# Optimization experiments

Measured on AMD Instinct MI355X. Metric: run time of the kernel, lower is better.

## Reference

```python
import jax, jax.numpy as jnp
import numpy as np

EMBED = 256
HEADS = 8
HEAD_DIM = 32
MLP_DIM = 1024
NEG = -1e9  # large negative in place of -inf so fully-deselected rows don't NaN
LN_EPS = 1e-5


def _layernorm(x, g, b):
    m = jnp.mean(x, axis=-1, keepdims=True)
    v = jnp.mean(jnp.square(x - m), axis=-1, keepdims=True)
    return (x - m) / jnp.sqrt(v + LN_EPS) * g + b


def setup_inputs() -> dict:
    key = jax.random.key(0)
    ks = jax.random.split(key, 16)
    b, s, d = 64, 360, EMBED
    sc = 0.02
    return {
        "x": jax.random.normal(ks[0], (b, s, d), dtype=jnp.float32),
        "attention_mask": jnp.zeros((b, 1, 1, s), dtype=jnp.float32),
        # TokenRouter.weight_predictor: Linear(256, 1)
        "wp_w": jax.random.normal(ks[1], (1, d), dtype=jnp.float32) * sc,
        "wp_b": jnp.zeros((1,), dtype=jnp.float32),
        # TokenRouter.aux_predictor: Linear(256,128) -> SiLU -> Linear(128,2)
        "a1_w": jax.random.normal(ks[2], (d // 2, d), dtype=jnp.float32) * sc,
        "a1_b": jnp.zeros((d // 2,), dtype=jnp.float32),
        "a2_w": jax.random.normal(ks[3], (2, d // 2), dtype=jnp.float32) * sc,
        "a2_b": jnp.zeros((2,), dtype=jnp.float32),
        # transformer block (pre-LN GPT2-style)
        "ln1_g": jnp.ones((d,), dtype=jnp.float32),
        "ln1_b": jnp.zeros((d,), dtype=jnp.float32),
        "wqkv": jax.random.normal(ks[4], (d, 3 * d), dtype=jnp.float32) * sc,
        "bqkv": jnp.zeros((3 * d,), dtype=jnp.float32),
        "wo": jax.random.normal(ks[5], (d, d), dtype=jnp.float32) * sc,
        "bo": jnp.zeros((d,), dtype=jnp.float32),
        "ln2_g": jnp.ones((d,), dtype=jnp.float32),
        "ln2_b": jnp.zeros((d,), dtype=jnp.float32),
        "w1": jax.random.normal(ks[6], (d, MLP_DIM), dtype=jnp.float32) * sc,
        "b1": jnp.zeros((MLP_DIM,), dtype=jnp.float32),
        "w2": jax.random.normal(ks[7], (MLP_DIM, d), dtype=jnp.float32) * sc,
        "b2": jnp.zeros((d,), dtype=jnp.float32),
    }


def reference(x, attention_mask, wp_w, wp_b, a1_w, a1_b, a2_w, a2_b,
              ln1_g, ln1_b, wqkv, bqkv, wo, bo, ln2_g, ln2_b, w1, b1, w2, b2):
    b, s, d = x.shape
    # --- router: per-token scalar weight ---
    weights = (x @ wp_w.T + wp_b).squeeze(-1)  # [b, s]
    # --- aux predictor selects tokens (eval path: argmax over 2 logits) ---
    h = jax.nn.silu(x @ a1_w.T + a1_b)
    aux_logits = h @ a2_w.T + a2_b            # [b, s, 2]
    sel = jnp.argmax(aux_logits, axis=-1).astype(bool)  # [b, s]
    # --- masked transformer block over the selected token subset.
    # Compacting tokens then attending == full-seq attention with deselected
    # keys masked out (LN/MLP/residual are position-wise), so vectorize:
    bias = attention_mask + jnp.where(sel, 0.0, NEG)[:, None, None, :]  # [b,1,1,s]
    hn = _layernorm(x, ln1_g, ln1_b)
    qkv = hn @ wqkv + bqkv
    q, k, v = jnp.split(qkv, 3, axis=-1)
    q = q.reshape(b, s, HEADS, HEAD_DIM)
    k = k.reshape(b, s, HEADS, HEAD_DIM)
    v = v.reshape(b, s, HEADS, HEAD_DIM)
    scores = jnp.einsum("bqhd,bkhd->bhqk", q, k) / np.sqrt(HEAD_DIM).astype(np.float32)
    scores = scores + bias                   # [b, h, s, s]
    attn = jax.nn.softmax(scores, axis=-1)
    ctx = jnp.einsum("bhqk,bkhd->bqhd", attn, v).reshape(b, s, d)
    h1 = x + (ctx @ wo + bo)
    h2n = _layernorm(h1, ln2_g, ln2_b)
    block_out = h1 + (jax.nn.gelu(h2n @ w1 + b1) @ w2 + b2)  # [b, s, d]
    # --- scatter-recombine: selected -> weighted block output, else passthrough
    out = jnp.where(sel[..., None], block_out * weights[..., None], x)
    avg_selected = jnp.sum(sel.astype(x.dtype)) / b
    return out, avg_selected
```

## Files before the change

kernel.cpp:

```cpp
#include <hip/hip_runtime.h>
#include <math.h>
#include <stdint.h>

#define TOKN 23040
#define BSZ 64
#define SEQ 360
#define DIM 256
#define NHD 8
#define HDD 32
#define MLPD 1024
#define NEGV -1e9f

typedef __attribute__((ext_vector_type(8))) short bf16x8;
typedef __attribute__((ext_vector_type(4))) float f32x4;

static __device__ __forceinline__ short f2bs(float f) {
  unsigned u = __builtin_bit_cast(unsigned, f);
  u += 0x7fffu + ((u >> 16) & 1u);
  return (short)(u >> 16);
}
static __device__ __forceinline__ float bf2f(short s) {
  unsigned u = ((unsigned)(unsigned short)s) << 16;
  return __builtin_bit_cast(float, u);
}
static __device__ __forceinline__ unsigned packbf(float a, float b) {
  return (unsigned)(unsigned short)f2bs(a) | ((unsigned)(unsigned short)f2bs(b) << 16);
}
static __device__ __forceinline__ void gl16(const short* g, short* l) {
  __builtin_amdgcn_global_load_lds(
      (const __attribute__((address_space(1))) unsigned int*)g,
      (__attribute__((address_space(3))) unsigned int*)l, 16, 0, 0);
}

__global__ __launch_bounds__(256) void convw_k(
    const float* __restrict__ wqkv, const float* __restrict__ wo,
    const float* __restrict__ w1, const float* __restrict__ w2,
    short* __restrict__ wqkvt, short* __restrict__ wot,
    short* __restrict__ w1t, short* __restrict__ w2t) {
  __shared__ float tile[32][33];
  int bid = blockIdx.x;
  const float* src;
  short* dst;
  int K, N, kt, nt;
  if (bid < 192) {
    src = wqkv; dst = wqkvt; K = 256; N = 768; kt = bid / 24; nt = bid % 24;
  } else if (bid < 256) {
    int b = bid - 192; src = wo; dst = wot; K = 256; N = 256; kt = b >> 3; nt = b & 7;
  } else if (bid < 512) {
    int b = bid - 256; src = w1; dst = w1t; K = 256; N = 1024; kt = b >> 5; nt = b & 31;
  } else {
    int b = bid - 512; src = w2; dst = w2t; K = 1024; N = 256; kt = b >> 3; nt = b & 7;
  }
  int t = threadIdx.x, r = t >> 3, c4 = (t & 7) * 4;
  const float4 v = *(const float4*)(src + (size_t)(kt * 32 + r) * N + nt * 32 + c4);
  tile[c4 + 0][r] = v.x;
  tile[c4 + 1][r] = v.y;
  tile[c4 + 2][r] = v.z;
  tile[c4 + 3][r] = v.w;
  __syncthreads();
  union { short s[4]; uint2 u; } o;
  o.s[0] = f2bs(tile[r][c4 + 0]);
  o.s[1] = f2bs(tile[r][c4 + 1]);
  o.s[2] = f2bs(tile[r][c4 + 2]);
  o.s[3] = f2bs(tile[r][c4 + 3]);
  *(uint2*)(dst + (size_t)(nt * 32 + r) * K + kt * 32 + c4) = o.u;
}

__global__ __launch_bounds__(256) void ln_router_k(
    const float* __restrict__ in, const float* __restrict__ g,
    const float* __restrict__ b, const float* __restrict__ wpw,
    const float* __restrict__ wpb, short* __restrict__ outn,
    float* __restrict__ wout, float* __restrict__ outx) {
  int tok = blockIdx.x * 4 + (threadIdx.x >> 6);
  int lane = threadIdx.x & 63;
  const float4 xv = *(const float4*)(in + (size_t)tok * DIM + lane * 4);
  *(float4*)(outx + (size_t)tok * DIM + lane * 4) = xv;
  float s = xv.x + xv.y + xv.z + xv.w;
  float s2 = xv.x * xv.x + xv.y * xv.y + xv.z * xv.z + xv.w * xv.w;
#pragma unroll
  for (int o = 1; o < 64; o <<= 1) { s += __shfl_xor(s, o); s2 += __shfl_xor(s2, o); }
  float m = s * (1.f / DIM);
  float var = fmaxf(s2 * (1.f / DIM) - m * m, 0.f);
  float rstd = rsqrtf(var + 1e-5f);
  float4 gv = *(const float4*)(g + lane * 4);
  float4 bv = *(const float4*)(b + lane * 4);
  uint2 pk;
  pk.x = packbf((xv.x - m) * rstd * gv.x + bv.x, (xv.y - m) * rstd * gv.y + bv.y);
  pk.y = packbf((xv.z - m) * rstd * gv.z + bv.z, (xv.w - m) * rstd * gv.w + bv.w);
  *(uint2*)(outn + (size_t)tok * DIM + lane * 4) = pk;
  float4 wv = *(const float4*)(wpw + lane * 4);
  float wd = xv.x * wv.x + xv.y * wv.y + xv.z * wv.z + xv.w * wv.w;
#pragma unroll
  for (int o = 1; o < 64; o <<= 1) wd += __shfl_xor(wd, o);
  if (lane == 0) wout[tok] = wd + wpb[0];
}

__global__ __launch_bounds__(256) void ln_k(
    const short* __restrict__ in, const float* __restrict__ g,
    const float* __restrict__ b, const int* __restrict__ mtotp,
    short* __restrict__ outn) {
  int tok = blockIdx.x * 4 + (threadIdx.x >> 6);
  int lane = threadIdx.x & 63;
  if (tok >= *mtotp) return;
  union { uint2 v; short s[4]; } u;
  u.v = *(const uint2*)(in + (size_t)tok * DIM + lane * 4);
  float x0 = bf2f(u.s[0]), x1 = bf2f(u.s[1]), x2 = bf2f(u.s[2]), x3 = bf2f(u.s[3]);
  float s = x0 + x1 + x2 + x3;
  float s2 = x0 * x0 + x1 * x1 + x2 * x2 + x3 * x3;
#pragma unroll
  for (int o = 1; o < 64; o <<= 1) { s += __shfl_xor(s, o); s2 += __shfl_xor(s2, o); }
  float m = s * (1.f / DIM);
  float var = fmaxf(s2 * (1.f / DIM) - m * m, 0.f);
  float rstd = rsqrtf(var + 1e-5f);
  float4 gv = *(const float4*)(g + lane * 4);
  float4 bv = *(const float4*)(b + lane * 4);
  uint2 pk;
  pk.x = packbf((x0 - m) * rstd * gv.x + bv.x, (x1 - m) * rstd * gv.y + bv.y);
  pk.y = packbf((x2 - m) * rstd * gv.z + bv.z, (x3 - m) * rstd * gv.w + bv.w);
  *(uint2*)(outn + (size_t)tok * DIM + lane * 4) = pk;
}

__global__ __launch_bounds__(256) void router_gemm_k(
    const float* __restrict__ x, const float* __restrict__ a1w,
    const float* __restrict__ a1b, const float* __restrict__ a2w,
    const float* __restrict__ a2b, int* __restrict__ sel) {
  __shared__ __align__(16) float XT[32][36];
  __shared__ __align__(16) float WT[32][128];
  int m0 = blockIdx.x * 32;
  int t = threadIdx.x;
  int tx = t & 31, ty = t >> 5;
  float acc[4][4] = {};
  int r = t >> 3, c = (t & 7) * 4;
  int n2 = t >> 1, c2 = (t & 1) * 16;
  for (int k0 = 0; k0 < 256; k0 += 32) {
    float4 xa = *(const float4*)(x + (size_t)(m0 + r) * 256 + k0 + c);
    XT[c + 0][r] = xa.x; XT[c + 1][r] = xa.y; XT[c + 2][r] = xa.z; XT[c + 3][r] = xa.w;
#pragma unroll
    for (int j = 0; j < 4; j++) {
      float4 wv = *(const float4*)(a1w + (size_t)n2 * 256 + k0 + c2 + j * 4);
      WT[c2 + j * 4 + 0][n2] = wv.x;
      WT[c2 + j * 4 + 1][n2] = wv.y;
      WT[c2 + j * 4 + 2][n2] = wv.z;
      WT[c2 + j * 4 + 3][n2] = wv.w;
    }
    __syncthreads();
#pragma unroll 8
    for (int kk = 0; kk < 32; kk++) {
      float4 wv4 = *(const float4*)&WT[kk][tx * 4];
      float4 xv4 = *(const float4*)&XT[kk][ty * 4];
      float xr[4] = {xv4.x, xv4.y, xv4.z, xv4.w};
      float wr[4] = {wv4.x, wv4.y, wv4.z, wv4.w};
#pragma unroll
      for (int i = 0; i < 4; i++)
#pragma unroll
        for (int j = 0; j < 4; j++) acc[i][j] += xr[i] * wr[j];
    }
    __syncthreads();
  }
  float b1v[4], a20[4], a21[4];
#pragma unroll
  for (int j = 0; j < 4; j++) {
    int dim = tx * 4 + j;
    b1v[j] = a1b[dim];
    a20[j] = a2w[dim];
    a21[j] = a2w[128 + dim];
  }
  float bias0 = a2b[0], bias1 = a2b[1];
#pragma unroll
  for (int i = 0; i < 4; i++) {
    float l0 = 0.f, l1 = 0.f;
#pragma unroll
    for (int j = 0; j < 4; j++) {
      float v = acc[i][j] + b1v[j];
      float h = v / (1.f + expf(-v));
      l0 += h * a20[j];
      l1 += h * a21[j];
    }
#pragma unroll
    for (int o = 1; o < 32; o <<= 1) { l0 += __shfl_xor(l0, o); l1 += __shfl_xor(l1, o); }
    if (tx == 0) sel[m0 + ty * 4 + i] = (l1 + bias1 > l0 + bias0) ? 1 : 0;
  }
}

__global__ __launch_bounds__(512) void scanA_k(const int* __restrict__ sel,
                                               int* __restrict__ idxl,
                                               int* __restrict__ cnt) {
  __shared__ int sc[512];
  int b = blockIdx.x, t = threadIdx.x;
  int flag = (t < SEQ) ? sel[b * SEQ + t] : 0;
  sc[t] = flag;
  __syncthreads();
  int val = flag;
  for (int off = 1; off < 512; off <<= 1) {
    int add = (t >= off) ? sc[t - off] : 0;
    __syncthreads();
    val += add;
    sc[t] = val;
    __syncthreads();
  }
  if (flag) idxl[b * SEQ + (val - 1)] = t;
  if (t == 511) cnt[b] = val;
}

__global__ __launch_bounds__(512) void scanB_k(const int* __restrict__ cnt,
                                               int* __restrict__ startp,
                                               int* __restrict__ mtotp,
                                               int* __restrict__ g_idx,
                                               float* __restrict__ outavg) {
  __shared__ int sc[64];
  __shared__ int mt;
  int t = threadIdx.x;
  if (t < 64) sc[t] = cnt[t];
  __syncthreads();
  if (t == 0) {
    int run = 0;
    for (int b = 0; b < 64; b++) { startp[b] = run; run += sc[b]; }
    *mtotp = run;
    mt = run;
    outavg[0] = (float)run / 64.0f;
  }
  __syncthreads();
  int m = mt;
  int e = m + 256;
  if (e > TOKN) e = TOKN;
  for (int i = m + t; i < e; i += 512) g_idx[i] = 0;
}

__global__ __launch_bounds__(512) void scanC_k(const int* __restrict__ idxl,
                                               const int* __restrict__ startp,
                                               const int* __restrict__ cnt,
                                               int* __restrict__ g_idx) {
  int b = blockIdx.x, t = threadIdx.x;
  int c = cnt[b], s0 = startp[b];
  for (int j = t; j < c; j += 512) g_idx[s0 + j] = b * SEQ + idxl[b * SEQ + j];
}

template <int MODE>
__global__ __launch_bounds__(256) void gemm_bt_k(
    const short* __restrict__ A, const short* __restrict__ Bt,
    const float* __restrict__ bias, const float* __restrict__ resf,
    const short* __restrict__ resb, const float* __restrict__ wgt,
    const int* __restrict__ g_idx, const int* __restrict__ mtotp,
    short* __restrict__ outb, float* __restrict__ outf, int Ndim, int Kdim) {
  int Mt = *mtotp;
  int m0 = blockIdx.y * 64;
  if (m0 >= Mt) return;
  __shared__ __align__(16) short As0[64 * 32];
  __shared__ __align__(16) short As1[64 * 32];
  __shared__ __align__(16) short Bs0[64 * 32];
  __shared__ __align__(16) short Bs1[64 * 32];
  int n0 = blockIdx.x * 64;
  int t = threadIdx.x;
  int wave = t >> 6, lane = t & 63;
  int l15 = lane & 15, quad = lane >> 4;
  int wr = (wave >> 1) * 32, wc = (wave & 1) * 32;
  int r0 = t >> 2, c0 = (t & 3) * 8;
  long ar0 = (MODE == 0) ? g_idx[m0 + r0] : (m0 + r0);
  const short* gA = A + ar0 * Kdim + c0;
  const short* gB = Bt + (size_t)(n0 + r0) * Kdim + c0;
  short* lA0 = As0 + wave * 512;
  short* lA1 = As1 + wave * 512;
  short* lB0 = Bs0 + wave * 512;
  short* lB1 = Bs1 + wave * 512;

  f32x4 acc[2][2];
#pragma unroll
  for (int i = 0; i < 2; i++)
#pragma unroll
    for (int j = 0; j < 2; j++)
#pragma unroll
      for (int r = 0; r < 4; r++) acc[i][j][r] = 0.f;

  for (int k0 = 0; k0 < Kdim; k0 += 64) {
    gl16(gA + k0, lA0);
    gl16(gA + k0 + 32, lA1);
    gl16(gB + k0, lB0);
    gl16(gB + k0 + 32, lB1);
    __syncthreads();
    bf16x8 a0[2], a1[2], b0[2], b1[2];
#pragma unroll
    for (int i = 0; i < 2; i++) {
      a0[i] = *(const bf16x8*)&As0[(wr + i * 16 + l15) * 32 + quad * 8];
      a1[i] = *(const bf16x8*)&As1[(wr + i * 16 + l15) * 32 + quad * 8];
      b0[i] = *(const bf16x8*)&Bs0[(wc + i * 16 + l15) * 32 + quad * 8];
      b1[i] = *(const bf16x8*)&Bs1[(wc + i * 16 + l15) * 32 + quad * 8];
    }
#pragma unroll
    for (int i = 0; i < 2; i++)
#pragma unroll
      for (int j = 0; j < 2; j++) {
        acc[i][j] = __builtin_amdgcn_mfma_f32_16x16x32_bf16(a0[i], b0[j],
                                                            acc[i][j], 0, 0, 0);
        acc[i][j] = __builtin_amdgcn_mfma_f32_16x16x32_bf16(a1[i], b1[j],
                                                            acc[i][j], 0, 0, 0);
      }
    __syncthreads();
  }

#pragma unroll
  for (int i = 0; i < 2; i++) {
#pragma unroll
    for (int j = 0; j < 2; j++) {
      int col = n0 + wc + j * 16 + l15;
      float bcol = bias[col];
#pragma unroll
      for (int r = 0; r < 4; r++) {
        int row = m0 + wr + i * 16 + quad * 4 + r;
        float v = acc[i][j][r] + bcol;
        size_t idx = (size_t)row * Ndim + col;
        if (MODE == 0) {
          outb[idx] = f2bs(v);
        } else if (MODE == 1) {
          int orig = g_idx[row];
          outb[idx] = f2bs(v + resf[(size_t)orig * 256 + col]);
        } else if (MODE == 2) {
          float u = 0.7978845608028654f * (v + 0.044715f * v * v * v);
          float e = __expf(2.f * u);
          float th = 1.f - 2.f / (e + 1.f);
          outb[idx] = f2bs(0.5f * v * (1.f + th));
        } else {
          if (row < Mt) {
            int orig = g_idx[row];
            float o = (v + bf2f(resb[idx])) * wgt[orig];
            outf[(size_t)orig * 256 + col] = o;
          }
        }
      }
    }
  }
}

template <int MODE, int BN>
__global__ __launch_bounds__(256) void gemm128_k(
    const short* __restrict__ A, const short* __restrict__ Bt,
    const float* __restrict__ bias, const float* __restrict__ resf,
    const short* __restrict__ resb, const float* __restrict__ wgt,
    const int* __restrict__ g_idx, const int* __restrict__ mtotp,
    short* __restrict__ outb, float* __restrict__ outf, int Ndim, int Kdim) {
  int Mt = *mtotp;
  int m0 = blockIdx.y * 128;
  if (m0 >= Mt) return;
  __shared__ __align__(16) short As0[128 * 32];
  __shared__ __align__(16) short As1[128 * 32];
  __shared__ __align__(16) short Bs0[BN * 32];
  __shared__ __align__(16) short Bs1[BN * 32];
  constexpr int NJ = BN / 32;
  int n0 = blockIdx.x * BN;
  int t = threadIdx.x;
  int wave = t >> 6, lane = t & 63;
  int l15 = lane & 15, quad = lane >> 4;
  int wr = (wave >> 1) * 64, wc = (wave & 1) * (BN / 2);
  int r0 = t >> 2, c0 = (t & 3) * 8;
  long arA = (MODE == 0) ? g_idx[m0 + r0] : (m0 + r0);
  long arB = (MODE == 0) ? g_idx[m0 + 64 + r0] : (m0 + 64 + r0);
  const short* gA0 = A + arA * Kdim + c0;
  const short* gA1 = A + arB * Kdim + c0;
  const short* gB0 = Bt + (size_t)(n0 + r0) * Kdim + c0;
  const short* gB1 = Bt + (size_t)(n0 + 64 + r0) * Kdim + c0;
  short* lA0 = As0 + wave * 512;
  short* lA1 = As1 + wave * 512;
  short* lB0 = Bs0 + wave * 512;
  short* lB1 = Bs1 + wave * 512;

  f32x4 acc[4][NJ];
#pragma unroll
  for (int i = 0; i < 4; i++)
#pragma unroll
    for (int j = 0; j < NJ; j++)
#pragma unroll
      for (int r = 0; r < 4; r++) acc[i][j][r] = 0.f;

  for (int k0 = 0; k0 < Kdim; k0 += 64) {
    gl16(gA0 + k0, lA0);
    gl16(gA1 + k0, lA0 + 2048);
    gl16(gA0 + k0 + 32, lA1);
    gl16(gA1 + k0 + 32, lA1 + 2048);
    gl16(gB0 + k0, lB0);
    gl16(gB0 + k0 + 32, lB1);
    if constexpr (BN == 128) {
      gl16(gB1 + k0, lB0 + 2048);
      gl16(gB1 + k0 + 32, lB1 + 2048);
    }
    __syncthreads();
    bf16x8 af[4], bfr[NJ];
#pragma unroll
    for (int i = 0; i < 4; i++)
      af[i] = *(const bf16x8*)&As0[(wr + i * 16 + l15) * 32 + quad * 8];
#pragma unroll
    for (int j = 0; j < NJ; j++)
      bfr[j] = *(const bf16x8*)&Bs0[(wc + j * 16 + l15) * 32 + quad * 8];
#pragma unroll
    for (int i = 0; i < 4; i++)
#pragma unroll
      for (int j = 0; j < NJ; j++)
        acc[i][j] = __builtin_amdgcn_mfma_f32_16x16x32_bf16(af[i], bfr[j],
                                                            acc[i][j], 0, 0, 0);
#pragma unroll
    for (int i = 0; i < 4; i++)
      af[i] = *(const bf16x8*)&As1[(wr + i * 16 + l15) * 32 + quad * 8];
#pragma unroll
    for (int j = 0; j < NJ; j++)
      bfr[j] = *(const bf16x8*)&Bs1[(wc + j * 16 + l15) * 32 + quad * 8];
#pragma unroll
    for (int i = 0; i < 4; i++)
#pragma unroll
      for (int j = 0; j < NJ; j++)
        acc[i][j] = __builtin_amdgcn_mfma_f32_16x16x32_bf16(af[i], bfr[j],
                                                            acc[i][j], 0, 0, 0);
    __syncthreads();
  }

#pragma unroll
  for (int i = 0; i < 4; i++) {
#pragma unroll
    for (int j = 0; j < NJ; j++) {
      int col = n0 + wc + j * 16 + l15;
      float bcol = bias[col];
#pragma unroll
      for (int r = 0; r < 4; r++) {
        int row = m0 + wr + i * 16 + quad * 4 + r;
        float v = acc[i][j][r] + bcol;
        size_t idx = (size_t)row * Ndim + col;
        if (MODE == 0) {
          outb[idx] = f2bs(v);
        } else if (MODE == 2) {
          float u = 0.7978845608028654f * (v + 0.044715f * v * v * v);
          float e = __expf(2.f * u);
          float th = 1.f - 2.f / (e + 1.f);
          outb[idx] = f2bs(0.5f * v * (1.f + th));
        } else {
          if (row < Mt) {
            int orig = g_idx[row];
            float o = (v + bf2f(resb[idx])) * wgt[orig];
            outf[(size_t)orig * 256 + col] = o;
          }
        }
      }
    }
  }
}

__global__ __launch_bounds__(256) void attn_k(
    const short* __restrict__ qkv, const float* __restrict__ amask,
    const int* __restrict__ g_idx, const int* __restrict__ startp,
    const int* __restrict__ cntp, short* __restrict__ ctx) {
  __shared__ __align__(16) short VF[2 * 12 * 64 * 8];
  __shared__ __align__(16) float ls[384];
  int bh = blockIdx.x >> 1, qhalf = blockIdx.x & 1;
  int bb = bh >> 3, h = bh & 7;
  int t = threadIdx.x;
  int start = startp[bb], cnt = cntp[bb];
  size_t base = (size_t)start * 768;
  for (int i = t; i < 1536; i += 256) {
    int k = i >> 2, cg = (i & 3) * 8;
    union { int4 v; short s[8]; } u;
    if (k < cnt) {
      u.v = *(const int4*)(qkv + base + (size_t)k * 768 + 512 + h * 32 + cg);
    } else {
      u.v = make_int4(0, 0, 0, 0);
    }
    int c = k >> 5, qd = (k >> 3) & 3, j = k & 7;
#pragma unroll
    for (int jj = 0; jj < 8; jj++) {
      int d = cg + jj;
      VF[((((d >> 4) * 12 + c) * 64) + qd * 16 + (d & 15)) * 8 + j] = u.s[jj];
    }
  }
  for (int i = t; i < 384; i += 256)
    ls[i] = (i < cnt) ? amask[g_idx[start + i]] : 0.f;
  __syncthreads();

  int wave = t >> 6, lane = t & 63;
  int ql = lane & 15, quad = lane >> 4;
  int addr0 = (((quad & 1) * 2) * 16 + ql) * 4;
  int addr1 = addr0 + 64;
  bool hiq = quad >= 2;
  int nt = (cnt + 15) >> 4;
  int nc = (cnt + 31) >> 5;

  for (int qt = qhalf + 2 * wave; qt < nt; qt += 8) {
    int q0 = qt * 16, qrow = q0 + ql;
    bf16x8 qf;
#pragma unroll
    for (int j = 0; j < 8; j++) qf[j] = 0;
    if (qrow < cnt)
      qf = *(const bf16x8*)(qkv + base + (size_t)qrow * 768 + h * 32 + quad * 8);

    f32x4 o0, o1;
#pragma unroll
    for (int r = 0; r < 4; r++) { o0[r] = 0.f; o1[r] = 0.f; }
    float lsum = 0.f;

    for (int c = 0; c < nc; c++) {
      int keyA = c * 32 + ql;
      int keyB = keyA + 16;
      bf16x8 kfA, kfB;
#pragma unroll
      for (int j = 0; j < 8; j++) { kfA[j] = 0; kfB[j] = 0; }
      if (keyA < cnt)
        kfA = *(const bf16x8*)(qkv + base + (size_t)keyA * 768 + 256 + h * 32 + quad * 8);
      if (keyB < cnt)
        kfB = *(const bf16x8*)(qkv + base + (size_t)keyB * 768 + 256 + h * 32 + quad * 8);
      f32x4 sa, sb;
#pragma unroll
      for (int r = 0; r < 4; r++) { sa[r] = 0.f; sb[r] = 0.f; }
      sa = __builtin_amdgcn_mfma_f32_16x16x32_bf16(kfA, qf, sa, 0, 0, 0);
      sb = __builtin_amdgcn_mfma_f32_16x16x32_bf16(kfB, qf, sb, 0, 0, 0);
      int kbase = c * 32 + quad * 4;
      float4 la = *(const float4*)&ls[kbase];
      float4 lb = *(const float4*)&ls[kbase + 16];
      float ea0 = (kbase + 0 < cnt) ? __expf(sa[0] * 0.17677669529663687f + la.x) : 0.f;
      float ea1 = (kbase + 1 < cnt) ? __expf(sa[1] * 0.17677669529663687f + la.y) : 0.f;
      float ea2 = (kbase + 2 < cnt) ? __expf(sa[2] * 0.17677669529663687f + la.z) : 0.f;
      float ea3 = (kbase + 3 < cnt) ? __expf(sa[3] * 0.17677669529663687f + la.w) : 0.f;
      float eb0 = (kbase + 16 < cnt) ? __expf(sb[0] * 0.17677669529663687f + lb.x) : 0.f;
      float eb1 = (kbase + 17 < cnt) ? __expf(sb[1] * 0.17677669529663687f + lb.y) : 0.f;
      float eb2 = (kbase + 18 < cnt) ? __expf(sb[2] * 0.17677669529663687f + lb.z) : 0.f;
      float eb3 = (kbase + 19 < cnt) ? __expf(sb[3] * 0.17677669529663687f + lb.w) : 0.f;
      lsum += (ea0 + ea1) + (ea2 + ea3) + (eb0 + eb1) + (eb2 + eb3);
      unsigned pA0 = packbf(ea0, ea1), pA1 = packbf(ea2, ea3);
      unsigned pB0 = packbf(eb0, eb1), pB1 = packbf(eb2, eb3);
      int s00 = __builtin_amdgcn_ds_bpermute(addr0, (int)pA0);
      int s10 = __builtin_amdgcn_ds_bpermute(addr0, (int)pB0);
      int s01 = __builtin_amdgcn_ds_bpermute(addr0, (int)pA1);
      int s11 = __builtin_amdgcn_ds_bpermute(addr0, (int)pB1);
      int s02 = __builtin_amdgcn_ds_bpermute(addr1, (int)pA0);
      int s12 = __builtin_amdgcn_ds_bpermute(addr1, (int)pB0);
      int s03 = __builtin_amdgcn_ds_bpermute(addr1, (int)pA1);
      int s13 = __builtin_amdgcn_ds_bpermute(addr1, (int)pB1);
      union { int i[4]; bf16x8 v; } pf;
      pf.i[0] = hiq ? s10 : s00;
      pf.i[1] = hiq ? s11 : s01;
      pf.i[2] = hiq ? s12 : s02;
      pf.i[3] = hiq ? s13 : s03;
      bf16x8 v0 = *(const bf16x8*)&VF[(c * 64 + lane) * 8];
      bf16x8 v1 = *(const bf16x8*)&VF[((12 + c) * 64 + lane) * 8];
      o0 = __builtin_amdgcn_mfma_f32_16x16x32_bf16(v0, pf.v, o0, 0, 0, 0);
      o1 = __builtin_amdgcn_mfma_f32_16x16x32_bf16(v1, pf.v, o1, 0, 0, 0);
    }
    lsum += __shfl_xor(lsum, 16);
    lsum += __shfl_xor(lsum, 32);
    float inv = 1.f / lsum;

    if (qrow < cnt) {
      size_t cb = ((size_t)(start + qrow)) * 256 + h * 32;
      uint2 w0, w1;
      w0.x = packbf(o0[0] * inv, o0[1] * inv);
      w0.y = packbf(o0[2] * inv, o0[3] * inv);
      w1.x = packbf(o1[0] * inv, o1[1] * inv);
      w1.y = packbf(o1[2] * inv, o1[3] * inv);
      *(uint2*)(ctx + cb + quad * 4) = w0;
      *(uint2*)(ctx + cb + 16 + quad * 4) = w1;
    }
  }
}

extern "C" void kernel_launch(void* const* d_in, const int* in_sizes, int n_in,
                              void* d_out, int out_size, void* d_ws,
                              size_t ws_size, hipStream_t stream) {
  const float* x = (const float*)d_in[0];
  const float* amask = (const float*)d_in[1];
  const float* wp_w = (const float*)d_in[2];
  const float* wp_b = (const float*)d_in[3];
  const float* a1_w = (const float*)d_in[4];
  const float* a1_b = (const float*)d_in[5];
  const float* a2_w = (const float*)d_in[6];
  const float* a2_b = (const float*)d_in[7];
  const float* ln1_g = (const float*)d_in[8];
  const float* ln1_b = (const float*)d_in[9];
  const float* wqkv = (const float*)d_in[10];
  const float* bqkv = (const float*)d_in[11];
  const float* wo = (const float*)d_in[12];
  const float* bo = (const float*)d_in[13];
  const float* ln2_g = (const float*)d_in[14];
  const float* ln2_b = (const float*)d_in[15];
  const float* w1 = (const float*)d_in[16];
  const float* b1 = (const float*)d_in[17];
  const float* w2 = (const float*)d_in[18];
  const float* b2 = (const float*)d_in[19];
  float* out = (float*)d_out;

  uint8_t* p = (uint8_t*)d_ws;
  float* weightsv = (float*)p; p += (size_t)TOKN * 4;
  int* selv = (int*)p;         p += (size_t)TOKN * 4;
  int* idxlv = (int*)p;        p += (size_t)TOKN * 4;
  int* gidxv = (int*)p;        p += (size_t)TOKN * 4;
  int* cntv = (int*)p;         p += 64 * 4;
  int* startv = (int*)p;       p += 64 * 4;
  int* mtotv = (int*)p;        p += 64 * 4;
  short* wqkvt = (short*)p;    p += (size_t)768 * 256 * 2;
  short* wot = (short*)p;      p += (size_t)256 * 256 * 2;
  short* w1t = (short*)p;      p += (size_t)1024 * 256 * 2;
  short* w2t = (short*)p;      p += (size_t)256 * 1024 * 2;
  short* h1bv = (short*)p;     p += (size_t)TOKN * 256 * 2;
  short* h2nv = (short*)p;     p += (size_t)TOKN * 256 * 2;
  short* ctxv = (short*)p;     p += (size_t)TOKN * 256 * 2;
  uint8_t* R = p;
  short* xnv = (short*)R;
  short* qkvv = (short*)(R + (size_t)TOKN * 256 * 2);
  short* actv = (short*)R;

  convw_k<<<dim3(768), dim3(256), 0, stream>>>(wqkv, wo, w1, w2, wqkvt, wot, w1t, w2t);
  ln_router_k<<<dim3(TOKN / 4), dim3(256), 0, stream>>>(x, ln1_g, ln1_b, wp_w, wp_b,
                                                        xnv, weightsv, out);
  router_gemm_k<<<dim3(720), dim3(256), 0, stream>>>(x, a1_w, a1_b, a2_w, a2_b, selv);
  scanA_k<<<dim3(64), dim3(512), 0, stream>>>(selv, idxlv, cntv);
  scanB_k<<<dim3(1), dim3(512), 0, stream>>>(cntv, startv, mtotv, gidxv,
                                             out + (size_t)TOKN * 256);
  scanC_k<<<dim3(64), dim3(512), 0, stream>>>(idxlv, startv, cntv, gidxv);
  gemm128_k<0, 128><<<dim3(6, 180), dim3(256), 0, stream>>>(
      xnv, wqkvt, bqkv, nullptr, nullptr, nullptr, gidxv, mtotv, qkvv, nullptr,
      768, 256);
  attn_k<<<dim3(1024), dim3(256), 0, stream>>>(qkvv, amask, gidxv, startv, cntv, ctxv);
  gemm_bt_k<1><<<dim3(4, 360), dim3(256), 0, stream>>>(
      ctxv, wot, bo, x, nullptr, nullptr, gidxv, mtotv, h1bv, nullptr, 256, 256);
  ln_k<<<dim3(TOKN / 4), dim3(256), 0, stream>>>(h1bv, ln2_g, ln2_b, mtotv, h2nv);
  gemm128_k<2, 128><<<dim3(8, 180), dim3(256), 0, stream>>>(
      h2nv, w1t, b1, nullptr, nullptr, nullptr, gidxv, mtotv, actv, nullptr,
      1024, 256);
  gemm128_k<3, 64><<<dim3(4, 180), dim3(256), 0, stream>>>(
      actv, w2t, b2, nullptr, h1bv, weightsv, gidxv, mtotv, nullptr, out, 256, 1024);
}
```

Before: 250.7 us.

## Merge prologue kernels, single-pass scan, fuse Wo GEMM with LayerNorm2

```diff
diff --git a/kernel.cpp b/kernel.cpp
--- a/kernel.cpp
+++ b/kernel.cpp
@@ -32,161 +32,150 @@
       (__attribute__((address_space(3))) unsigned int*)l, 16, 0, 0);
 }
 
-__global__ __launch_bounds__(256) void convw_k(
+__global__ __launch_bounds__(256) void mega_k(
+    const float* __restrict__ x, const float* __restrict__ g,
+    const float* __restrict__ b, const float* __restrict__ wpw,
+    const float* __restrict__ wpb, short* __restrict__ outn,
+    float* __restrict__ wout, float* __restrict__ outx,
+    const float* __restrict__ a1w, const float* __restrict__ a1b,
+    const float* __restrict__ a2w, const float* __restrict__ a2b,
+    int* __restrict__ sel,
     const float* __restrict__ wqkv, const float* __restrict__ wo,
     const float* __restrict__ w1, const float* __restrict__ w2,
     short* __restrict__ wqkvt, short* __restrict__ wot,
     short* __restrict__ w1t, short* __restrict__ w2t) {
-  __shared__ float tile[32][33];
+  __shared__ __align__(16) unsigned char smem[20992];
   int bid = blockIdx.x;
-  const float* src;
-  short* dst;
-  int K, N, kt, nt;
-  if (bid < 192) {
-    src = wqkv; dst = wqkvt; K = 256; N = 768; kt = bid / 24; nt = bid % 24;
-  } else if (bid < 256) {
-    int b = bid - 192; src = wo; dst = wot; K = 256; N = 256; kt = b >> 3; nt = b & 7;
-  } else if (bid < 512) {
-    int b = bid - 256; src = w1; dst = w1t; K = 256; N = 1024; kt = b >> 5; nt = b & 31;
+  int t = threadIdx.x;
+
+  if (bid < 720) {
+    float(*XT)[36] = (float(*)[36])smem;
+    float(*WT)[128] = (float(*)[128])(smem + 4608);
+    int m0 = bid * 32;
+    int tx = t & 31, ty = t >> 5;
+    float acc[4][4] = {};
+    int r = t >> 3, c = (t & 7) * 4;
+    int n2 = t >> 1, c2 = (t & 1) * 16;
+    for (int k0 = 0; k0 < 256; k0 += 32) {
+      float4 xa = *(const float4*)(x + (size_t)(m0 + r) * 256 + k0 + c);
+      XT[c + 0][r] = xa.x; XT[c + 1][r] = xa.y; XT[c + 2][r] = xa.z; XT[c + 3][r] = xa.w;
+#pragma unroll
+      for (int j = 0; j < 4; j++) {
+        float4 wv = *(const float4*)(a1w + (size_t)n2 * 256 + k0 + c2 + j * 4);
+        WT[c2 + j * 4 + 0][n2] = wv.x;
+        WT[c2 + j * 4 + 1][n2] = wv.y;
+        WT[c2 + j * 4 + 2][n2] = wv.z;
+        WT[c2 + j * 4 + 3][n2] = wv.w;
+      }
+      __syncthreads();
+#pragma unroll 8
+      for (int kk = 0; kk < 32; kk++) {
+        float4 wv4 = *(const float4*)&WT[kk][tx * 4];
+        float4 xv4 = *(const float4*)&XT[kk][ty * 4];
+        float xr[4] = {xv4.x, xv4.y, xv4.z, xv4.w};
+        float wr[4] = {wv4.x, wv4.y, wv4.z, wv4.w};
+#pragma unroll
+        for (int i = 0; i < 4; i++)
+#pragma unroll
+          for (int j = 0; j < 4; j++) acc[i][j] += xr[i] * wr[j];
+      }
+      __syncthreads();
+    }
+    float b1v[4], a20[4], a21[4];
+#pragma unroll
+    for (int j = 0; j < 4; j++) {
+      int dim = tx * 4 + j;
+      b1v[j] = a1b[dim];
+      a20[j] = a2w[dim];
+      a21[j] = a2w[128 + dim];
+    }
+    float bias0 = a2b[0], bias1 = a2b[1];
+#pragma unroll
+    for (int i = 0; i < 4; i++) {
+      float l0 = 0.f, l1 = 0.f;
+#pragma unroll
+      for (int j = 0; j < 4; j++) {
+        float v = acc[i][j] + b1v[j];
+        float h = v / (1.f + expf(-v));
+        l0 += h * a20[j];
+        l1 += h * a21[j];
+      }
+#pragma unroll
+      for (int o = 1; o < 32; o <<= 1) { l0 += __shfl_xor(l0, o); l1 += __shfl_xor(l1, o); }
+      if (tx == 0) sel[m0 + ty * 4 + i] = (l1 + bias1 > l0 + bias0) ? 1 : 0;
+    }
+  } else if (bid < 1488) {
+    float(*tile)[33] = (float(*)[33])smem;
+    int b2 = bid - 720;
+    const float* src;
+    short* dst;
+    int K, N, kt, nt;
+    if (b2 < 192) {
+      src = wqkv; dst = wqkvt; K = 256; N = 768; kt = b2 / 24; nt = b2 % 24;
+    } else if (b2 < 256) {
+      int bb = b2 - 192; src = wo; dst = wot; K = 256; N = 256; kt = bb >> 3; nt = bb & 7;
+    } else if (b2 < 512) {
+      int bb = b2 - 256; src = w1; dst = w1t; K = 256; N = 1024; kt = bb >> 5; nt = bb & 31;
+    } else {
+      int bb = b2 - 512; src = w2; dst = w2t; K = 1024; N = 256; kt = bb >> 3; nt = bb & 7;
+    }
+    int r = t >> 3, c4 = (t & 7) * 4;
+    const float4 v = *(const float4*)(src + (size_t)(kt * 32 + r) * N + nt * 32 + c4);
+    tile[c4 + 0][r] = v.x;
+    tile[c4 + 1][r] = v.y;
+    tile[c4 + 2][r] = v.z;
+    tile[c4 + 3][r] = v.w;
+    __syncthreads();
+    union { short s[4]; uint2 u; } o;
+    o.s[0] = f2bs(tile[r][c4 + 0]);
+    o.s[1] = f2bs(tile[r][c4 + 1]);
+    o.s[2] = f2bs(tile[r][c4 + 2]);
+    o.s[3] = f2bs(tile[r][c4 + 3]);
+    *(uint2*)(dst + (size_t)(nt * 32 + r) * K + kt * 32 + c4) = o.u;
   } else {
-    int b = bid - 512; src = w2; dst = w2t; K = 1024; N = 256; kt = b >> 3; nt = b & 7;
-  }
-  int t = threadIdx.x, r = t >> 3, c4 = (t & 7) * 4;
-  const float4 v = *(const float4*)(src + (size_t)(kt * 32 + r) * N + nt * 32 + c4);
-  tile[c4 + 0][r] = v.x;
-  tile[c4 + 1][r] = v.y;
-  tile[c4 + 2][r] = v.z;
-  tile[c4 + 3][r] = v.w;
+    int tok = (bid - 1488) * 4 + (t >> 6);
+    int lane = t & 63;
+    const float4 xv = *(const float4*)(x + (size_t)tok * DIM + lane * 4);
+    *(float4*)(outx + (size_t)tok * DIM + lane * 4) = xv;
+    float s = xv.x + xv.y + xv.z + xv.w;
+    float s2 = xv.x * xv.x + xv.y * xv.y + xv.z * xv.z + xv.w * xv.w;
+#pragma unroll
+    for (int o = 1; o < 64; o <<= 1) { s += __shfl_xor(s, o); s2 += __shfl_xor(s2, o); }
+    float m = s * (1.f / DIM);
+    float var = fmaxf(s2 * (1.f / DIM) - m * m, 0.f);
+    float rstd = rsqrtf(var + 1e-5f);
+    float4 gv = *(const float4*)(g + lane * 4);
+    float4 bv = *(const float4*)(b + lane * 4);
+    uint2 pk;
+    pk.x = packbf((xv.x - m) * rstd * gv.x + bv.x, (xv.y - m) * rstd * gv.y + bv.y);
+    pk.y = packbf((xv.z - m) * rstd * gv.z + bv.z, (xv.w - m) * rstd * gv.w + bv.w);
+    *(uint2*)(outn + (size_t)tok * DIM + lane * 4) = pk;
+    float4 wv = *(const float4*)(wpw + lane * 4);
+    float wd = xv.x * wv.x + xv.y * wv.y + xv.z * wv.z + xv.w * wv.w;
+#pragma unroll
+    for (int o = 1; o < 64; o <<= 1) wd += __shfl_xor(wd, o);
+    if (lane == 0) wout[tok] = wd + wpb[0];
+  }
+}
+
+__global__ __launch_bounds__(512) void scan_k(
+    const int* __restrict__ sel, int* __restrict__ g_idx,
+    int* __restrict__ startp, int* __restrict__ cntp,
+    int* __restrict__ mtotp, float* __restrict__ outavg) {
+  __shared__ int sc[512];
+  __shared__ int red[8];
+  int b = blockIdx.x, t = threadIdx.x;
+  int lane = t & 63, wave = t >> 6;
+  int part = 0;
+  for (int i = t; i < b * SEQ; i += 512) part += sel[i];
+#pragma unroll
+  for (int o = 1; o < 64; o <<= 1) part += __shfl_xor(part, o);
+  if (lane == 0) red[wave] = part;
   __syncthreads();
-  union { short s[4]; uint2 u; } o;
-  o.s[0] = f2bs(tile[r][c4 + 0]);
-  o.s[1] = f2bs(tile[r][c4 + 1]);
-  o.s[2] = f2bs(tile[r][c4 + 2]);
-  o.s[3] = f2bs(tile[r][c4 + 3]);
-  *(uint2*)(dst + (size_t)(nt * 32 + r) * K + kt * 32 + c4) = o.u;
-}
-
-__global__ __launch_bounds__(256) void ln_router_k(
-    const float* __restrict__ in, const float* __restrict__ g,
-    const float* __restrict__ b, const float* __restrict__ wpw,
-    const float* __restrict__ wpb, short* __restrict__ outn,
-    float* __restrict__ wout, float* __restrict__ outx) {
-  int tok = blockIdx.x * 4 + (threadIdx.x >> 6);
-  int lane = threadIdx.x & 63;
-  const float4 xv = *(const float4*)(in + (size_t)tok * DIM + lane * 4);
-  *(float4*)(outx + (size_t)tok * DIM + lane * 4) = xv;
-  float s = xv.x + xv.y + xv.z + xv.w;
-  float s2 = xv.x * xv.x + xv.y * xv.y + xv.z * xv.z + xv.w * xv.w;
-#pragma unroll
-  for (int o = 1; o < 64; o <<= 1) { s += __shfl_xor(s, o); s2 += __shfl_xor(s2, o); }
-  float m = s * (1.f / DIM);
-  float var = fmaxf(s2 * (1.f / DIM) - m * m, 0.f);
-  float rstd = rsqrtf(var + 1e-5f);
-  float4 gv = *(const float4*)(g + lane * 4);
-  float4 bv = *(const float4*)(b + lane * 4);
-  uint2 pk;
-  pk.x = packbf((xv.x - m) * rstd * gv.x + bv.x, (xv.y - m) * rstd * gv.y + bv.y);
-  pk.y = packbf((xv.z - m) * rstd * gv.z + bv.z, (xv.w - m) * rstd * gv.w + bv.w);
-  *(uint2*)(outn + (size_t)tok * DIM + lane * 4) = pk;
-  float4 wv = *(const float4*)(wpw + lane * 4);
-  float wd = xv.x * wv.x + xv.y * wv.y + xv.z * wv.z + xv.w * wv.w;
-#pragma unroll
-  for (int o = 1; o < 64; o <<= 1) wd += __shfl_xor(wd, o);
-  if (lane == 0) wout[tok] = wd + wpb[0];
-}
-
-__global__ __launch_bounds__(256) void ln_k(
-    const short* __restrict__ in, const float* __restrict__ g,
-    const float* __restrict__ b, const int* __restrict__ mtotp,
-    short* __restrict__ outn) {
-  int tok = blockIdx.x * 4 + (threadIdx.x >> 6);
-  int lane = threadIdx.x & 63;
-  if (tok >= *mtotp) return;
-  union { uint2 v; short s[4]; } u;
-  u.v = *(const uint2*)(in + (size_t)tok * DIM + lane * 4);
-  float x0 = bf2f(u.s[0]), x1 = bf2f(u.s[1]), x2 = bf2f(u.s[2]), x3 = bf2f(u.s[3]);
-  float s = x0 + x1 + x2 + x3;
-  float s2 = x0 * x0 + x1 * x1 + x2 * x2 + x3 * x3;
-#pragma unroll
-  for (int o = 1; o < 64; o <<= 1) { s += __shfl_xor(s, o); s2 += __shfl_xor(s2, o); }
-  float m = s * (1.f / DIM);
-  float var = fmaxf(s2 * (1.f / DIM) - m * m, 0.f);
-  float rstd = rsqrtf(var + 1e-5f);
-  float4 gv = *(const float4*)(g + lane * 4);
-  float4 bv = *(const float4*)(b + lane * 4);
-  uint2 pk;
-  pk.x = packbf((x0 - m) * rstd * gv.x + bv.x, (x1 - m) * rstd * gv.y + bv.y);
-  pk.y = packbf((x2 - m) * rstd * gv.z + bv.z, (x3 - m) * rstd * gv.w + bv.w);
-  *(uint2*)(outn + (size_t)tok * DIM + lane * 4) = pk;
-}
-
-__global__ __launch_bounds__(256) void router_gemm_k(
-    const float* __restrict__ x, const float* __restrict__ a1w,
-    const float* __restrict__ a1b, const float* __restrict__ a2w,
-    const float* __restrict__ a2b, int* __restrict__ sel) {
-  __shared__ __align__(16) float XT[32][36];
-  __shared__ __align__(16) float WT[32][128];
-  int m0 = blockIdx.x * 32;
-  int t = threadIdx.x;
-  int tx = t & 31, ty = t >> 5;
-  float acc[4][4] = {};
-  int r = t >> 3, c = (t & 7) * 4;
-  int n2 = t >> 1, c2 = (t & 1) * 16;
-  for (int k0 = 0; k0 < 256; k0 += 32) {
-    float4 xa = *(const float4*)(x + (size_t)(m0 + r) * 256 + k0 + c);
-    XT[c + 0][r] = xa.x; XT[c + 1][r] = xa.y; XT[c + 2][r] = xa.z; XT[c + 3][r] = xa.w;
-#pragma unroll
-    for (int j = 0; j < 4; j++) {
-      float4 wv = *(const float4*)(a1w + (size_t)n2 * 256 + k0 + c2 + j * 4);
-      WT[c2 + j * 4 + 0][n2] = wv.x;
-      WT[c2 + j * 4 + 1][n2] = wv.y;
-      WT[c2 + j * 4 + 2][n2] = wv.z;
-      WT[c2 + j * 4 + 3][n2] = wv.w;
-    }
-    __syncthreads();
-#pragma unroll 8
-    for (int kk = 0; kk < 32; kk++) {
-      float4 wv4 = *(const float4*)&WT[kk][tx * 4];
-      float4 xv4 = *(const float4*)&XT[kk][ty * 4];
-      float xr[4] = {xv4.x, xv4.y, xv4.z, xv4.w};
-      float wr[4] = {wv4.x, wv4.y, wv4.z, wv4.w};
-#pragma unroll
-      for (int i = 0; i < 4; i++)
-#pragma unroll
-        for (int j = 0; j < 4; j++) acc[i][j] += xr[i] * wr[j];
-    }
-    __syncthreads();
-  }
-  float b1v[4], a20[4], a21[4];
-#pragma unroll
-  for (int j = 0; j < 4; j++) {
-    int dim = tx * 4 + j;
-    b1v[j] = a1b[dim];
-    a20[j] = a2w[dim];
-    a21[j] = a2w[128 + dim];
-  }
-  float bias0 = a2b[0], bias1 = a2b[1];
-#pragma unroll
-  for (int i = 0; i < 4; i++) {
-    float l0 = 0.f, l1 = 0.f;
-#pragma unroll
-    for (int j = 0; j < 4; j++) {
-      float v = acc[i][j] + b1v[j];
-      float h = v / (1.f + expf(-v));
-      l0 += h * a20[j];
-      l1 += h * a21[j];
-    }
-#pragma unroll
-    for (int o = 1; o < 32; o <<= 1) { l0 += __shfl_xor(l0, o); l1 += __shfl_xor(l1, o); }
-    if (tx == 0) sel[m0 + ty * 4 + i] = (l1 + bias1 > l0 + bias0) ? 1 : 0;
-  }
-}
-
-__global__ __launch_bounds__(512) void scanA_k(const int* __restrict__ sel,
-                                               int* __restrict__ idxl,
-                                               int* __restrict__ cnt) {
-  __shared__ int sc[512];
-  int b = blockIdx.x, t = threadIdx.x;
+  int start = 0;
+#pragma unroll
+  for (int w = 0; w < 8; w++) start += red[w];
+  __syncthreads();
   int flag = (t < SEQ) ? sel[b * SEQ + t] : 0;
   sc[t] = flag;
   __syncthreads();
@@ -198,135 +187,14 @@
     sc[t] = val;
     __syncthreads();
   }
-  if (flag) idxl[b * SEQ + (val - 1)] = t;
-  if (t == 511) cnt[b] = val;
-}
-
-__global__ __launch_bounds__(512) void scanB_k(const int* __restrict__ cnt,
-                                               int* __restrict__ startp,
-                                               int* __restrict__ mtotp,
-                                               int* __restrict__ g_idx,
-                                               float* __restrict__ outavg) {
-  __shared__ int sc[64];
-  __shared__ int mt;
-  int t = threadIdx.x;
-  if (t < 64) sc[t] = cnt[t];
-  __syncthreads();
-  if (t == 0) {
-    int run = 0;
-    for (int b = 0; b < 64; b++) { startp[b] = run; run += sc[b]; }
-    *mtotp = run;
-    mt = run;
-    outavg[0] = (float)run / 64.0f;
-  }
-  __syncthreads();
-  int m = mt;
-  int e = m + 256;
-  if (e > TOKN) e = TOKN;
-  for (int i = m + t; i < e; i += 512) g_idx[i] = 0;
-}
-
-__global__ __launch_bounds__(512) void scanC_k(const int* __restrict__ idxl,
-                                               const int* __restrict__ startp,
-                                               const int* __restrict__ cnt,
-                                               int* __restrict__ g_idx) {
-  int b = blockIdx.x, t = threadIdx.x;
-  int c = cnt[b], s0 = startp[b];
-  for (int j = t; j < c; j += 512) g_idx[s0 + j] = b * SEQ + idxl[b * SEQ + j];
-}
-
-template <int MODE>
-__global__ __launch_bounds__(256) void gemm_bt_k(
-    const short* __restrict__ A, const short* __restrict__ Bt,
-    const float* __restrict__ bias, const float* __restrict__ resf,
-    const short* __restrict__ resb, const float* __restrict__ wgt,
-    const int* __restrict__ g_idx, const int* __restrict__ mtotp,
-    short* __restrict__ outb, float* __restrict__ outf, int Ndim, int Kdim) {
-  int Mt = *mtotp;
-  int m0 = blockIdx.y * 64;
-  if (m0 >= Mt) return;
-  __shared__ __align__(16) short As0[64 * 32];
-  __shared__ __align__(16) short As1[64 * 32];
-  __shared__ __align__(16) short Bs0[64 * 32];
-  __shared__ __align__(16) short Bs1[64 * 32];
-  int n0 = blockIdx.x * 64;
-  int t = threadIdx.x;
-  int wave = t >> 6, lane = t & 63;
-  int l15 = lane & 15, quad = lane >> 4;
-  int wr = (wave >> 1) * 32, wc = (wave & 1) * 32;
-  int r0 = t >> 2, c0 = (t & 3) * 8;
-  long ar0 = (MODE == 0) ? g_idx[m0 + r0] : (m0 + r0);
-  const short* gA = A + ar0 * Kdim + c0;
-  const short* gB = Bt + (size_t)(n0 + r0) * Kdim + c0;
-  short* lA0 = As0 + wave * 512;
-  short* lA1 = As1 + wave * 512;
-  short* lB0 = Bs0 + wave * 512;
-  short* lB1 = Bs1 + wave * 512;
-
-  f32x4 acc[2][2];
-#pragma unroll
-  for (int i = 0; i < 2; i++)
-#pragma unroll
-    for (int j = 0; j < 2; j++)
-#pragma unroll
-      for (int r = 0; r < 4; r++) acc[i][j][r] = 0.f;
-
-  for (int k0 = 0; k0 < Kdim; k0 += 64) {
-    gl16(gA + k0, lA0);
-    gl16(gA + k0 + 32, lA1);
-    gl16(gB + k0, lB0);
-    gl16(gB + k0 + 32, lB1);
-    __syncthreads();
-    bf16x8 a0[2], a1[2], b0[2], b1[2];
-#pragma unroll
-    for (int i = 0; i < 2; i++) {
-      a0[i] = *(const bf16x8*)&As0[(wr + i * 16 + l15) * 32 + quad * 8];
-      a1[i] = *(const bf16x8*)&As1[(wr + i * 16 + l15) * 32 + quad * 8];
-      b0[i] = *(const bf16x8*)&Bs0[(wc + i * 16 + l15) * 32 + quad * 8];
-      b1[i] = *(const bf16x8*)&Bs1[(wc + i * 16 + l15) * 32 + quad * 8];
-    }
-#pragma unroll
-    for (int i = 0; i < 2; i++)
-#pragma unroll
-      for (int j = 0; j < 2; j++) {
-        acc[i][j] = __builtin_amdgcn_mfma_f32_16x16x32_bf16(a0[i], b0[j],
-                                                            acc[i][j], 0, 0, 0);
-        acc[i][j] = __builtin_amdgcn_mfma_f32_16x16x32_bf16(a1[i], b1[j],
-                                                            acc[i][j], 0, 0, 0);
-      }
-    __syncthreads();
-  }
-
-#pragma unroll
-  for (int i = 0; i < 2; i++) {
-#pragma unroll
-    for (int j = 0; j < 2; j++) {
-      int col = n0 + wc + j * 16 + l15;
-      float bcol = bias[col];
-#pragma unroll
-      for (int r = 0; r < 4; r++) {
-        int row = m0 + wr + i * 16 + quad * 4 + r;
-        float v = acc[i][j][r] + bcol;
-        size_t idx = (size_t)row * Ndim + col;
-        if (MODE == 0) {
-          outb[idx] = f2bs(v);
-        } else if (MODE == 1) {
-          int orig = g_idx[row];
-          outb[idx] = f2bs(v + resf[(size_t)orig * 256 + col]);
-        } else if (MODE == 2) {
-          float u = 0.7978845608028654f * (v + 0.044715f * v * v * v);
-          float e = __expf(2.f * u);
-          float th = 1.f - 2.f / (e + 1.f);
-          outb[idx] = f2bs(0.5f * v * (1.f + th));
-        } else {
-          if (row < Mt) {
-            int orig = g_idx[row];
-            float o = (v + bf2f(resb[idx])) * wgt[orig];
-            outf[(size_t)orig * 256 + col] = o;
-          }
-        }
-      }
-    }
+  if (flag) g_idx[start + val - 1] = b * SEQ + t;
+  if (t == 511) { startp[b] = start; cntp[b] = val; }
+  if (b == 63) {
+    int mt = start + sc[511];
+    if (t == 0) { *mtotp = mt; outavg[0] = (float)mt / 64.0f; }
+    int e = mt + 256;
+    if (e > TOKN) e = TOKN;
+    for (int i = mt + t; i < e; i += 512) g_idx[i] = 0;
   }
 }
 
@@ -435,6 +303,152 @@
             outf[(size_t)orig * 256 + col] = o;
           }
         }
+      }
+    }
+  }
+}
+
+__global__ __launch_bounds__(256) void wo_ln_k(
+    const short* __restrict__ A, const short* __restrict__ Bt,
+    const float* __restrict__ bias, const float* __restrict__ resf,
+    const float* __restrict__ g2, const float* __restrict__ b2,
+    const int* __restrict__ g_idx, const int* __restrict__ mtotp,
+    short* __restrict__ h1b, short* __restrict__ h2n) {
+  int Mt = *mtotp;
+  int m0 = blockIdx.x * 128;
+  if (m0 >= Mt) return;
+  __shared__ __align__(16) short As0[128 * 32];
+  __shared__ __align__(16) short As1[128 * 32];
+  __shared__ __align__(16) short Bs0[256 * 32];
+  __shared__ __align__(16) short Bs1[256 * 32];
+  __shared__ float ps[128][2], ps2[128][2];
+  int t = threadIdx.x;
+  int wave = t >> 6, lane = t & 63;
+  int l15 = lane & 15, quad = lane >> 4;
+  int wr = (wave >> 1) * 64, wc = (wave & 1) * 128;
+  int r0 = t >> 2, c0 = (t & 3) * 8;
+  const short* gA0 = A + (size_t)(m0 + r0) * 256 + c0;
+  const short* gA1 = A + (size_t)(m0 + 64 + r0) * 256 + c0;
+  const short* gB0 = Bt + (size_t)r0 * 256 + c0;
+  short* lA0 = As0 + wave * 512;
+  short* lA1 = As1 + wave * 512;
+  short* lB0 = Bs0 + wave * 512;
+  short* lB1 = Bs1 + wave * 512;
+
+  f32x4 acc[4][8];
+#pragma unroll
+  for (int i = 0; i < 4; i++)
+#pragma unroll
+    for (int j = 0; j < 8; j++)
+#pragma unroll
+      for (int r = 0; r < 4; r++) acc[i][j][r] = 0.f;
+
+  for (int k0 = 0; k0 < 256; k0 += 64) {
+    gl16(gA0 + k0, lA0);
+    gl16(gA1 + k0, lA0 + 2048);
+    gl16(gA0 + k0 + 32, lA1);
+    gl16(gA1 + k0 + 32, lA1 + 2048);
+#pragma unroll
+    for (int q = 0; q < 4; q++) {
+      gl16(gB0 + (size_t)q * 64 * 256 + k0, lB0 + q * 2048);
+      gl16(gB0 + (size_t)q * 64 * 256 + k0 + 32, lB1 + q * 2048);
+    }
+    __syncthreads();
+    bf16x8 af[4], bfr[8];
+#pragma unroll
+    for (int i = 0; i < 4; i++)
+      af[i] = *(const bf16x8*)&As0[(wr + i * 16 + l15) * 32 + quad * 8];
+#pragma unroll
+    for (int j = 0; j < 8; j++)
+      bfr[j] = *(const bf16x8*)&Bs0[(wc + j * 16 + l15) * 32 + quad * 8];
+#pragma unroll
+    for (int i = 0; i < 4; i++)
+#pragma unroll
+      for (int j = 0; j < 8; j++)
+        acc[i][j] = __builtin_amdgcn_mfma_f32_16x16x32_bf16(af[i], bfr[j],
+                                                            acc[i][j], 0, 0, 0);
+#pragma unroll
+    for (int i = 0; i < 4; i++)
+      af[i] = *(const bf16x8*)&As1[(wr + i * 16 + l15) * 32 + quad * 8];
+#pragma unroll
+    for (int j = 0; j < 8; j++)
+      bfr[j] = *(const bf16x8*)&Bs1[(wc + j * 16 + l15) * 32 + quad * 8];
+#pragma unroll
+    for (int i = 0; i < 4; i++)
+#pragma unroll
+      for (int j = 0; j < 8; j++)
+        acc[i][j] = __builtin_amdgcn_mfma_f32_16x16x32_bf16(af[i], bfr[j],
+                                                            acc[i][j], 0, 0, 0);
+    __syncthreads();
+  }
+
+  float bcol[8], gcol[8], bbcol[8];
+#pragma unroll
+  for (int j = 0; j < 8; j++) {
+    int col = wc + j * 16 + l15;
+    bcol[j] = bias[col];
+    gcol[j] = g2[col];
+    bbcol[j] = b2[col];
+  }
+  float s1v[4][4], s2v[4][4];
+#pragma unroll
+  for (int i = 0; i < 4; i++) {
+#pragma unroll
+    for (int r = 0; r < 4; r++) {
+      int row = m0 + wr + i * 16 + quad * 4 + r;
+      int orig = g_idx[row];
+      const float* xr = resf + (size_t)orig * 256;
+      float ls_ = 0.f, ls2_ = 0.f;
+#pragma unroll
+      for (int j = 0; j < 8; j++) {
+        int col = wc + j * 16 + l15;
+        float h1 = acc[i][j][r] + bcol[j] + xr[col];
+        acc[i][j][r] = h1;
+        h1b[(size_t)row * 256 + col] = f2bs(h1);
+        ls_ += h1;
+        ls2_ += h1 * h1;
+      }
+      s1v[i][r] = ls_;
+      s2v[i][r] = ls2_;
+    }
+  }
+#pragma unroll
+  for (int i = 0; i < 4; i++)
+#pragma unroll
+    for (int r = 0; r < 4; r++) {
+#pragma unroll
+      for (int o = 1; o < 16; o <<= 1) {
+        s1v[i][r] += __shfl_xor(s1v[i][r], o);
+        s2v[i][r] += __shfl_xor(s2v[i][r], o);
+      }
+    }
+  if (l15 == 0) {
+#pragma unroll
+    for (int i = 0; i < 4; i++)
+#pragma unroll
+      for (int r = 0; r < 4; r++) {
+        int lr = wr + i * 16 + quad * 4 + r;
+        ps[lr][wave & 1] = s1v[i][r];
+        ps2[lr][wave & 1] = s2v[i][r];
+      }
+  }
+  __syncthreads();
+#pragma unroll
+  for (int i = 0; i < 4; i++) {
+#pragma unroll
+    for (int r = 0; r < 4; r++) {
+      int lr = wr + i * 16 + quad * 4 + r;
+      float S = ps[lr][0] + ps[lr][1];
+      float S2 = ps2[lr][0] + ps2[lr][1];
+      float m = S * (1.f / 256.f);
+      float var = fmaxf(S2 * (1.f / 256.f) - m * m, 0.f);
+      float rstd = rsqrtf(var + 1e-5f);
+      int row = m0 + lr;
+#pragma unroll
+      for (int j = 0; j < 8; j++) {
+        int col = wc + j * 16 + l15;
+        float h2 = (acc[i][j][r] - m) * rstd * gcol[j] + bbcol[j];
+        h2n[(size_t)row * 256 + col] = f2bs(h2);
       }
     }
   }
@@ -599,22 +613,20 @@
   short* xnv = (short*)R;
   short* qkvv = (short*)(R + (size_t)TOKN * 256 * 2);
   short* actv = (short*)R;
-
-  convw_k<<<dim3(768), dim3(256), 0, stream>>>(wqkv, wo, w1, w2, wqkvt, wot, w1t, w2t);
-  ln_router_k<<<dim3(TOKN / 4), dim3(256), 0, stream>>>(x, ln1_g, ln1_b, wp_w, wp_b,
-                                                        xnv, weightsv, out);
-  router_gemm_k<<<dim3(720), dim3(256), 0, stream>>>(x, a1_w, a1_b, a2_w, a2_b, selv);
-  scanA_k<<<dim3(64), dim3(512), 0, stream>>>(selv, idxlv, cntv);
-  scanB_k<<<dim3(1), dim3(512), 0, stream>>>(cntv, startv, mtotv, gidxv,
+  (void)idxlv;
+
+  mega_k<<<dim3(7248), dim3(256), 0, stream>>>(
+      x, ln1_g, ln1_b, wp_w, wp_b, xnv, weightsv, out,
+      a1_w, a1_b, a2_w, a2_b, selv,
+      wqkv, wo, w1, w2, wqkvt, wot, w1t, w2t);
+  scan_k<<<dim3(64), dim3(512), 0, stream>>>(selv, gidxv, startv, cntv, mtotv,
                                              out + (size_t)TOKN * 256);
-  scanC_k<<<dim3(64), dim3(512), 0, stream>>>(idxlv, startv, cntv, gidxv);
   gemm128_k<0, 128><<<dim3(6, 180), dim3(256), 0, stream>>>(
       xnv, wqkvt, bqkv, nullptr, nullptr, nullptr, gidxv, mtotv, qkvv, nullptr,
       768, 256);
   attn_k<<<dim3(1024), dim3(256), 0, stream>>>(qkvv, amask, gidxv, startv, cntv, ctxv);
-  gemm_bt_k<1><<<dim3(4, 360), dim3(256), 0, stream>>>(
-      ctxv, wot, bo, x, nullptr, nullptr, gidxv, mtotv, h1bv, nullptr, 256, 256);
-  ln_k<<<dim3(TOKN / 4), dim3(256), 0, stream>>>(h1bv, ln2_g, ln2_b, mtotv, h2nv);
+  wo_ln_k<<<dim3(180), dim3(256), 0, stream>>>(ctxv, wot, bo, x, ln2_g, ln2_b,
+                                               gidxv, mtotv, h1bv, h2nv);
   gemm128_k<2, 128><<<dim3(8, 180), dim3(256), 0, stream>>>(
       h2nv, w1t, b1, nullptr, nullptr, nullptr, gidxv, mtotv, actv, nullptr,
       1024, 256);
```

After: 253.5 us. No clear change (+1.1%).
